# Optimization experiments

Measured on AMD Instinct MI355X. Metric: run time of the kernel, lower is better.

Reference implementation:

```python
import jax, jax.numpy as jnp
import numpy as np

EMBED = 1024
HIDDEN = 4 * EMBED
EPS = 1e-5

def _layer_norm(x, g, b):
    mu = jnp.mean(x, axis=-1, keepdims=True)
    var = jnp.mean((x - mu) ** 2, axis=-1, keepdims=True)
    return (x - mu) * jax.lax.rsqrt(var + EPS) * g + b

def setup_inputs() -> dict:
    key = jax.random.key(0)
    ks = jax.random.split(key, 8)
    s = 1.0 / np.sqrt(EMBED)
    inp = {
        "x": jax.random.normal(ks[0], (4, 2048, EMBED), dtype=jnp.float32),
        "Wq": jax.random.normal(ks[1], (EMBED, EMBED), dtype=jnp.float32) * s,
        "bq": jnp.zeros((EMBED,), jnp.float32),
        "Wk": jax.random.normal(ks[2], (EMBED, EMBED), dtype=jnp.float32) * s,
        "bk": jnp.zeros((EMBED,), jnp.float32),
        "Wv": jax.random.normal(ks[3], (EMBED, EMBED), dtype=jnp.float32) * s,
        "bv": jnp.zeros((EMBED,), jnp.float32),
        "W1": jax.random.normal(ks[4], (EMBED, HIDDEN), dtype=jnp.float32) * s,
        "b1": jnp.zeros((HIDDEN,), jnp.float32),
        "W2": jax.random.normal(ks[5], (HIDDEN, EMBED), dtype=jnp.float32) * (1.0 / np.sqrt(HIDDEN)),
        "b2": jnp.zeros((EMBED,), jnp.float32),
        "g1": jnp.ones((EMBED,), jnp.float32),
        "be1": jnp.zeros((EMBED,), jnp.float32),
        "g2": jnp.ones((EMBED,), jnp.float32),
        "be2": jnp.zeros((EMBED,), jnp.float32),
    }
    return inp

def reference(x, Wq, bq, Wk, bk, Wv, bv, W1, b1, W2, b2, g1, be1, g2, be2):
    # pre-norm attention
    h = _layer_norm(x, g1, be1)
    Q = h @ Wq + bq  # [B,S,D]
    K = h @ Wk + bk
    V = h @ Wv + bv
    scale = 1.0 / jnp.sqrt(jnp.asarray(EMBED, x.dtype))
    scores = jnp.einsum('bqd,bkd->bqk', Q, K) * scale  # [B,S,S]
    weights = jax.nn.softmax(scores, axis=-1)
    attn = jnp.einsum('bqk,bkd->bqd', weights, V)
    x = x + attn
    # pre-norm MLP
    h2 = _layer_norm(x, g2, be2)
    ff = jax.nn.relu(h2 @ W1 + b1) @ W2 + b2
    return x + ff
```

## Files before the change

### kernel.cpp

```cpp
#include <hip/hip_runtime.h>

#define EMBED 1024
#define HID   4096
#define NB    4
#define SEQ   2048

typedef __attribute__((ext_vector_type(8)))  __bf16 bf16x8;
typedef __attribute__((ext_vector_type(4)))  float  f32x4;
typedef __attribute__((ext_vector_type(4)))  int    i32x4;
typedef unsigned short u16;

__device__ __forceinline__ u16 f2bf(float f) {
  unsigned u = __float_as_uint(f);
  u += 0x7FFFu + ((u >> 16) & 1u);
  return (u16)(u >> 16);
}
__device__ __forceinline__ float bf2f(u16 u) {
  return __uint_as_float(((unsigned)u) << 16);
}

typedef const __attribute__((address_space(1))) unsigned int* gas_t;
typedef __attribute__((address_space(3))) unsigned int* las_t;
__device__ __forceinline__ void gld16(const void* g, void* l) {
  __builtin_amdgcn_global_load_lds((gas_t)g, (las_t)l, 16, 0, 0);
}

#define RD16(p)       __builtin_bit_cast(bf16x8, *(const i32x4*)(p))
#define MFMA16(a,b,c) __builtin_amdgcn_mfma_f32_16x16x32_bf16(a, b, c, 0, 0, 0)
#define SCHED0()      __builtin_amdgcn_sched_barrier(0)
#define BARR()        __builtin_amdgcn_s_barrier()
#define LGKM(n)       asm volatile("s_waitcnt lgkmcnt(" #n ")" ::: "memory")
#define VMW(n)        asm volatile("s_waitcnt vmcnt(" #n ")" ::: "memory")

template<int EPI>
__global__ __launch_bounds__(512, 2) void gemm256(
    const u16* __restrict__ A, int lda, long long astr,
    const u16* __restrict__ B, int ldb, long long bstr,
    void* __restrict__ C, int ldc, long long cstr,
    const float* __restrict__ bias,
    const float* __restrict__ add,
    float scale, int Kdim)
{
  __shared__ char lds[131072];

  const int tid  = threadIdx.x;
  const int lane = tid & 63;
  const int w    = tid >> 6;
  const int wr   = w >> 2, wc = w & 3;
  const int l15  = lane & 15, l4 = lane >> 4;

  const int gx   = gridDim.x;
  const int nwg  = gx * gridDim.y;
  const int orig = blockIdx.y * gx + blockIdx.x;
  const int t    = ((nwg & 7) == 0) ? ((orig & 7) * (nwg >> 3) + (orig >> 3)) : orig;
  const int bx   = t % gx, by = t / gx;

  const u16* Ab = A + (size_t)blockIdx.z * astr + (size_t)by * 256 * lda;
  const u16* Bb = B + (size_t)blockIdx.z * bstr + (size_t)bx * 256 * ldb;

  const int    srow = tid >> 3;
  const size_t sa   = (size_t)srow * lda + (size_t)(((tid & 7) ^ (srow & 7)) * 8);
  const size_t sb   = (size_t)srow * ldb + (size_t)(((tid & 7) ^ (srow & 7)) * 8);
  const int    ldst = tid * 16;

  auto stA = [&](int buf, int q, int kk) {
    gld16(Ab + (size_t)(q * 64) * lda + kk + sa, lds + buf * 65536 + q * 8192 + ldst);
  };
  auto stB = [&](int buf, int i, int kk) {
    gld16(Bb + (size_t)(i * 64) * ldb + kk + sb, lds + buf * 65536 + 32768 + i * 8192 + ldst);
  };

  const int arow = (wr * 128 + l15) * 128;
  const int brow = 32768 + (wc * 64 + l15) * 128;
  const int cp0  = ((0 + l4) ^ (l15 & 7)) * 16;
  const int cp1  = ((4 + l4) ^ (l15 & 7)) * 16;

  f32x4 acc[8][4] = {};
  bf16x8 a0, a1, a2, a3, b0, b1, b2, b3, b4, b5, b6, b7;

  const int NT = Kdim >> 6;
  const int NI = NT >> 1;

#define BLOADS(LB) \
    b0 = RD16((LB) + brow + 0 * 2048 + cp0); \
    b1 = RD16((LB) + brow + 1 * 2048 + cp0); \
    b2 = RD16((LB) + brow + 2 * 2048 + cp0); \
    b3 = RD16((LB) + brow + 3 * 2048 + cp0); \
    b4 = RD16((LB) + brow + 0 * 2048 + cp1); \
    b5 = RD16((LB) + brow + 1 * 2048 + cp1); \
    b6 = RD16((LB) + brow + 2 * 2048 + cp1); \
    b7 = RD16((LB) + brow + 3 * 2048 + cp1);

#define PHASE(LB, MP, PRE, STG, VMST) do { \
    a0 = RD16((LB) + arow + (MP) * 4096 + cp0); \
    a1 = RD16((LB) + arow + (MP) * 4096 + cp1); \
    a2 = RD16((LB) + arow + (MP) * 4096 + 2048 + cp0); \
    a3 = RD16((LB) + arow + (MP) * 4096 + 2048 + cp1); \
    PRE STG VMST \
    SCHED0(); BARR(); LGKM(0); SCHED0(); \
    __builtin_amdgcn_s_setprio(1); \
    acc[2*(MP)  ][0] = MFMA16(a0, b0, acc[2*(MP)  ][0]); \
    acc[2*(MP)  ][1] = MFMA16(a0, b1, acc[2*(MP)  ][1]); \
    acc[2*(MP)  ][2] = MFMA16(a0, b2, acc[2*(MP)  ][2]); \
    acc[2*(MP)  ][3] = MFMA16(a0, b3, acc[2*(MP)  ][3]); \
    acc[2*(MP)+1][0] = MFMA16(a2, b0, acc[2*(MP)+1][0]); \
    acc[2*(MP)+1][1] = MFMA16(a2, b1, acc[2*(MP)+1][1]); \
    acc[2*(MP)+1][2] = MFMA16(a2, b2, acc[2*(MP)+1][2]); \
    acc[2*(MP)+1][3] = MFMA16(a2, b3, acc[2*(MP)+1][3]); \
    acc[2*(MP)  ][0] = MFMA16(a1, b4, acc[2*(MP)  ][0]); \
    acc[2*(MP)  ][1] = MFMA16(a1, b5, acc[2*(MP)  ][1]); \
    acc[2*(MP)  ][2] = MFMA16(a1, b6, acc[2*(MP)  ][2]); \
    acc[2*(MP)  ][3] = MFMA16(a1, b7, acc[2*(MP)  ][3]); \
    acc[2*(MP)+1][0] = MFMA16(a3, b4, acc[2*(MP)+1][0]); \
    acc[2*(MP)+1][1] = MFMA16(a3, b5, acc[2*(MP)+1][1]); \
    acc[2*(MP)+1][2] = MFMA16(a3, b6, acc[2*(MP)+1][2]); \
    acc[2*(MP)+1][3] = MFMA16(a3, b7, acc[2*(MP)+1][3]); \
    __builtin_amdgcn_s_setprio(0); \
    SCHED0(); BARR(); SCHED0(); \
  } while (0)

  stB(0, 0, 0); stB(0, 1, 0); stB(0, 2, 0); stB(0, 3, 0);
  stA(0, 0, 0); stA(0, 1, 0); stA(0, 2, 0); stA(0, 3, 0);
  stB(1, 0, 64); stB(1, 1, 64); stB(1, 2, 64); stB(1, 3, 64);
  stA(1, 0, 64); stA(1, 2, 64);
  VMW(6);
  BARR(); SCHED0();

  const char* L0 = lds;
  const char* L1 = lds + 65536;

  for (int I = 0; I < NI; ++I) {
    const bool st = (I + 1 < NI);
    const int k1 = (2 * I + 1) * 64;
    const int k2 = (2 * I + 2) * 64;
    const int k3 = (2 * I + 3) * 64;

    PHASE(L0, 0, BLOADS(L0), { stA(1, 1, k1); stA(1, 3, k1); }, ;);
    PHASE(L0, 1, ;, if (st) { stB(0, 0, k2); stB(0, 1, k2); }, ;);
    PHASE(L0, 2, ;, if (st) { stB(0, 2, k2); stB(0, 3, k2); }, ;);
    if (st) { PHASE(L0, 3, ;, { stA(0, 0, k2); stA(0, 2, k2); }, VMW(6);); }
    else    { PHASE(L0, 3, ;, ;, VMW(0);); }
    PHASE(L1, 0, BLOADS(L1), if (st) { stA(0, 1, k2); stA(0, 3, k2); }, ;);
    PHASE(L1, 1, ;, if (st) { stB(1, 0, k3); stB(1, 1, k3); }, ;);
    PHASE(L1, 2, ;, if (st) { stB(1, 2, k3); stB(1, 3, k3); }, ;);
    if (st) { PHASE(L1, 3, ;, { stA(1, 0, k3); stA(1, 2, k3); }, VMW(6);); }
    else    { PHASE(L1, 3, ;, ;, ;); }
  }
#undef PHASE
#undef BLOADS

  const int bm0 = by * 256 + wr * 128;
  const int bn0 = bx * 256 + wc * 64;
  float* Cf = (float*)C;
  u16*   Ch = (u16*)C;
  #pragma unroll
  for (int mi = 0; mi < 8; ++mi) {
    #pragma unroll
    for (int ni = 0; ni < 4; ++ni) {
      const int col = bn0 + ni * 16 + l15;
      const int r0  = bm0 + mi * 16 + l4 * 4;
      float bv = 0.f;
      if (EPI == 0 || EPI == 3 || EPI == 4) bv = bias[col];
      #pragma unroll
      for (int r = 0; r < 4; ++r) {
        const size_t idx = (size_t)blockIdx.z * cstr + (size_t)(r0 + r) * ldc + col;
        const float v = acc[mi][ni][r];
        if      (EPI == 0) Ch[idx] = f2bf(v + bv);
        else if (EPI == 1) Cf[idx] = v * scale;
        else if (EPI == 3) Ch[idx] = f2bf(fmaxf(v + bv, 0.f));
        else if (EPI == 4) Cf[idx] = v + bv + add[idx];
      }
    }
  }
}

template<int EPI>
__global__ __launch_bounds__(512, 2) void gemm8p(
    const u16* __restrict__ A, int lda, long long astr,
    const u16* __restrict__ B, int ldb, long long bstr,
    void* __restrict__ C, int ldc, long long cstr,
    const float* __restrict__ bias,
    const float* __restrict__ add,
    float scale, int Kdim)
{
  __shared__ i32x4 lds4[9216];
  const int SLOT = 49152;

  const int tid  = threadIdx.x;
  const int lane = tid & 63;
  const int w    = tid >> 6;
  const int wr   = w >> 1, wc = w & 1;
  const int l15  = lane & 15, l4 = lane >> 4;

  const int gx   = gridDim.x;
  const int nwg  = gx * gridDim.y;
  const int orig = blockIdx.y * gx + blockIdx.x;
  const int t    = ((nwg & 7) == 0) ? ((orig & 7) * (nwg >> 3) + (orig >> 3)) : orig;
  const int bx   = t % gx, by = t / gx;

  const u16* Ab = A + (size_t)blockIdx.z * astr + (size_t)by * 256 * lda;
  const u16* Bb = B + (size_t)blockIdx.z * bstr + (size_t)bx * 128 * ldb;

  size_t gaoff[4], gboff[2];
  #pragma unroll
  for (int i = 0; i < 4; ++i) {
    const int idx = i * 512 + tid, row = idx >> 3, gc = (idx & 7) ^ (row & 7);
    gaoff[i] = (size_t)row * lda + gc * 8;
  }
  #pragma unroll
  for (int j = 0; j < 2; ++j) {
    const int idx = j * 512 + tid, row = idx >> 3, gc = (idx & 7) ^ (row & 7);
    gboff[j] = (size_t)row * ldb + gc * 8;
  }

  int aoff[4], boff[4], cp16[2];
  #pragma unroll
  for (int m = 0; m < 4; ++m) aoff[m] = (wr * 64 + m * 16 + l15) * 128;
  #pragma unroll
  for (int n = 0; n < 4; ++n) boff[n] = 32768 + (wc * 64 + n * 16 + l15) * 128;
  cp16[0] = ((0 + l4) ^ (l15 & 7)) * 16;
  cp16[1] = ((4 + l4) ^ (l15 & 7)) * 16;

  f32x4 acc[4][4] = {};
  const int NT = Kdim >> 6;
  char* lbase = (char*)lds4;

  {
    char* s0 = lbase;
    char* s1 = lbase + SLOT;
    #pragma unroll
    for (int i = 0; i < 4; ++i) gld16(Ab + gaoff[i],      s0 + (i * 512 + w * 64) * 16);
    #pragma unroll
    for (int j = 0; j < 2; ++j) gld16(Bb + gboff[j],      s0 + 32768 + (j * 512 + w * 64) * 16);
    #pragma unroll
    for (int i = 0; i < 4; ++i) gld16(Ab + gaoff[i] + 64, s1 + (i * 512 + w * 64) * 16);
    #pragma unroll
    for (int j = 0; j < 2; ++j) gld16(Bb + gboff[j] + 64, s1 + 32768 + (j * 512 + w * 64) * 16);
  }

  int s = 0;
  for (int T = 0; T < NT; ++T) {
    const bool st  = (T + 2 < NT);
    const size_t kk = (size_t)(T + 2) * 64;
    const char* rA = lbase + s * SLOT;
    char* wS = lbase + ((s + 2 >= 3) ? (s - 1) : (s + 2)) * SLOT;

    if (T == NT - 1) VMW(0);
    else             VMW(6);
    BARR();
    SCHED0();

    bf16x8 b0, b1, b2, b3, a0, a1;

    b0 = RD16(rA + boff[0] + cp16[0]);
    b1 = RD16(rA + boff[1] + cp16[0]);
    b2 = RD16(rA + boff[2] + cp16[0]);
    b3 = RD16(rA + boff[3] + cp16[0]);
    a0 = RD16(rA + aoff[0] + cp16[0]);
    a1 = RD16(rA + aoff[1] + cp16[0]);
    if (st) {
      gld16(Ab + gaoff[0] + kk, wS + (0 * 512 + w * 64) * 16);
      gld16(Ab + gaoff[1] + kk, wS + (1 * 512 + w * 64) * 16);
    }
    BARR();
    LGKM(0);
    SCHED0();
    __builtin_amdgcn_s_setprio(1);
    acc[0][0] = MFMA16(a0, b0, acc[0][0]);
    acc[0][1] = MFMA16(a0, b1, acc[0][1]);
    acc[0][2] = MFMA16(a0, b2, acc[0][2]);
    acc[0][3] = MFMA16(a0, b3, acc[0][3]);
    acc[1][0] = MFMA16(a1, b0, acc[1][0]);
    acc[1][1] = MFMA16(a1, b1, acc[1][1]);
    acc[1][2] = MFMA16(a1, b2, acc[1][2]);
    acc[1][3] = MFMA16(a1, b3, acc[1][3]);
    __builtin_amdgcn_s_setprio(0);

    a0 = RD16(rA + aoff[2] + cp16[0]);
    a1 = RD16(rA + aoff[3] + cp16[0]);
    if (st) {
      gld16(Ab + gaoff[2] + kk, wS + (2 * 512 + w * 64) * 16);
      gld16(Ab + gaoff[3] + kk, wS + (3 * 512 + w * 64) * 16);
    }
    BARR();
    LGKM(0);
    SCHED0();
    __builtin_amdgcn_s_setprio(1);
    acc[2][0] = MFMA16(a0, b0, acc[2][0]);
    acc[2][1] = MFMA16(a0, b1, acc[2][1]);
    acc[2][2] = MFMA16(a0, b2, acc[2][2]);
    acc[2][3] = MFMA16(a0, b3, acc[2][3]);
    acc[3][0] = MFMA16(a1, b0, acc[3][0]);
    acc[3][1] = MFMA16(a1, b1, acc[3][1]);
    acc[3][2] = MFMA16(a1, b2, acc[3][2]);
    acc[3][3] = MFMA16(a1, b3, acc[3][3]);
    __builtin_amdgcn_s_setprio(0);

    b0 = RD16(rA + boff[0] + cp16[1]);
    b1 = RD16(rA + boff[1] + cp16[1]);
    b2 = RD16(rA + boff[2] + cp16[1]);
    b3 = RD16(rA + boff[3] + cp16[1]);
    a0 = RD16(rA + aoff[0] + cp16[1]);
    a1 = RD16(rA + aoff[1] + cp16[1]);
    if (st) {
      gld16(Bb + gboff[0] + kk, wS + 32768 + (0 * 512 + w * 64) * 16);
    }
    BARR();
    LGKM(0);
    SCHED0();
    __builtin_amdgcn_s_setprio(1);
    acc[0][0] = MFMA16(a0, b0, acc[0][0]);
    acc[0][1] = MFMA16(a0, b1, acc[0][1]);
    acc[0][2] = MFMA16(a0, b2, acc[0][2]);
    acc[0][3] = MFMA16(a0, b3, acc[0][3]);
    acc[1][0] = MFMA16(a1, b0, acc[1][0]);
    acc[1][1] = MFMA16(a1, b1, acc[1][1]);
    acc[1][2] = MFMA16(a1, b2, acc[1][2]);
    acc[1][3] = MFMA16(a1, b3, acc[1][3]);
    __builtin_amdgcn_s_setprio(0);

    a0 = RD16(rA + aoff[2] + cp16[1]);
    a1 = RD16(rA + aoff[3] + cp16[1]);
    if (st) {
      gld16(Bb + gboff[1] + kk, wS + 32768 + (1 * 512 + w * 64) * 16);
    }
    BARR();
    LGKM(0);
    SCHED0();
    __builtin_amdgcn_s_setprio(1);
    acc[2][0] = MFMA16(a0, b0, acc[2][0]);
    acc[2][1] = MFMA16(a0, b1, acc[2][1]);
    acc[2][2] = MFMA16(a0, b2, acc[2][2]);
    acc[2][3] = MFMA16(a0, b3, acc[2][3]);
    acc[3][0] = MFMA16(a1, b0, acc[3][0]);
    acc[3][1] = MFMA16(a1, b1, acc[3][1]);
    acc[3][2] = MFMA16(a1, b2, acc[3][2]);
    acc[3][3] = MFMA16(a1, b3, acc[3][3]);
    __builtin_amdgcn_s_setprio(0);

    s = (s + 1 == 3) ? 0 : s + 1;
  }

  const int bm0 = by * 256 + wr * 64;
  const int bn0 = bx * 128 + wc * 64;
  float* Cf = (float*)C;
  u16*   Ch = (u16*)C;
  #pragma unroll
  for (int mi = 0; mi < 4; ++mi) {
    #pragma unroll
    for (int ni = 0; ni < 4; ++ni) {
      const int col = bn0 + ni * 16 + l15;
      const int r0  = bm0 + mi * 16 + l4 * 4;
      float bv = 0.f;
      if (EPI == 0 || EPI == 4) bv = bias[col];
      #pragma unroll
      for (int r = 0; r < 4; ++r) {
        const size_t idx = (size_t)blockIdx.z * cstr + (size_t)(r0 + r) * ldc + col;
        const float v = acc[mi][ni][r];
        if      (EPI == 0) Ch[idx] = f2bf(v + bv);
        else if (EPI == 1) Cf[idx] = v * scale;
        else if (EPI == 2) Cf[idx] = v + add[idx];
        else if (EPI == 4) Cf[idx] = v + bv + add[idx];
        else if (EPI == 5) Ch[idx] = f2bf(v + bias[r0 + r]);
        else if (EPI == 6) Ch[idx] = f2bf(v * scale);
      }
    }
  }
}

__global__ __launch_bounds__(256) void ln_kernel(
    const float* __restrict__ x, const float* __restrict__ g,
    const float* __restrict__ be, u16* __restrict__ out)
{
  const int row = blockIdx.x;
  const int tid = threadIdx.x;
  const float4 v = ((const float4*)(x + (size_t)row * EMBED))[tid];
  float s  = v.x + v.y + v.z + v.w;
  float s2 = v.x * v.x + v.y * v.y + v.z * v.z + v.w * v.w;
  #pragma unroll
  for (int m = 1; m < 64; m <<= 1) { s += __shfl_xor(s, m); s2 += __shfl_xor(s2, m); }
  __shared__ float ls[4], ls2[4];
  const int w = tid >> 6;
  if ((tid & 63) == 0) { ls[w] = s; ls2[w] = s2; }
  __syncthreads();
  s  = ls[0] + ls[1] + ls[2] + ls[3];
  s2 = ls2[0] + ls2[1] + ls2[2] + ls2[3];
  const float mu   = s * (1.f / EMBED);
  const float var  = s2 * (1.f / EMBED) - mu * mu;
  const float rstd = rsqrtf(var + 1e-5f);
  const float4 gv = ((const float4*)g)[tid];
  const float4 bv = ((const float4*)be)[tid];
  ushort4 o;
  o.x = f2bf((v.x - mu) * rstd * gv.x + bv.x);
  o.y = f2bf((v.y - mu) * rstd * gv.y + bv.y);
  o.z = f2bf((v.z - mu) * rstd * gv.z + bv.z);
  o.w = f2bf((v.w - mu) * rstd * gv.w + bv.w);
  ((ushort4*)(out + (size_t)row * EMBED))[tid] = o;
}

__global__ __launch_bounds__(256) void softmax_bf16(
    const u16* __restrict__ S, u16* __restrict__ P)
{
  const int tid = threadIdx.x;
  const size_t base = ((size_t)blockIdx.y * SEQ + blockIdx.x) * SEQ;
  const ushort4* src = (const ushort4*)(S + base);
  const ushort4 ua = src[tid];
  const ushort4 ub = src[tid + 256];
  float a0 = bf2f(ua.x), a1 = bf2f(ua.y), a2 = bf2f(ua.z), a3 = bf2f(ua.w);
  float b0 = bf2f(ub.x), b1 = bf2f(ub.y), b2 = bf2f(ub.z), b3 = bf2f(ub.w);
  float m = fmaxf(fmaxf(fmaxf(a0, a1), fmaxf(a2, a3)),
                  fmaxf(fmaxf(b0, b1), fmaxf(b2, b3)));
  #pragma unroll
  for (int msk = 1; msk < 64; msk <<= 1) m = fmaxf(m, __shfl_xor(m, msk));
  __shared__ float red[8];
  const int w = tid >> 6;
  if ((tid & 63) == 0) red[w] = m;
  __syncthreads();
  m = fmaxf(fmaxf(red[0], red[1]), fmaxf(red[2], red[3]));
  a0 = __expf(a0 - m); a1 = __expf(a1 - m); a2 = __expf(a2 - m); a3 = __expf(a3 - m);
  b0 = __expf(b0 - m); b1 = __expf(b1 - m); b2 = __expf(b2 - m); b3 = __expf(b3 - m);
  float s = a0 + a1 + a2 + a3 + b0 + b1 + b2 + b3;
  #pragma unroll
  for (int msk = 1; msk < 64; msk <<= 1) s += __shfl_xor(s, msk);
  if ((tid & 63) == 0) red[4 + w] = s;
  __syncthreads();
  s = red[4] + red[5] + red[6] + red[7];
  const float inv = 1.0f / s;
  ushort4 oa, ob;
  oa.x = f2bf(a0 * inv); oa.y = f2bf(a1 * inv); oa.z = f2bf(a2 * inv); oa.w = f2bf(a3 * inv);
  ob.x = f2bf(b0 * inv); ob.y = f2bf(b1 * inv); ob.z = f2bf(b2 * inv); ob.w = f2bf(b3 * inv);
  ushort4* dst = (ushort4*)(P + base);
  dst[tid]       = oa;
  dst[tid + 256] = ob;
}

__global__ void transpose_cast3(const float* __restrict__ W0,
                                const float* __restrict__ W1_,
                                const float* __restrict__ W2_,
                                u16* __restrict__ Wt)
{
  __shared__ float t[32][33];
  const int z = blockIdx.z;
  const float* W = (z == 0) ? W0 : (z == 1) ? W1_ : W2_;
  u16* dst = Wt + (size_t)z * EMBED * EMBED;
  const int tx = threadIdx.x, ty = threadIdx.y;
  const int n0 = blockIdx.x * 32, k0 = blockIdx.y * 32;
  #pragma unroll
  for (int i = 0; i < 4; ++i)
    t[ty + i * 8][tx] = W[(size_t)(k0 + ty + i * 8) * EMBED + n0 + tx];
  __syncthreads();
  #pragma unroll
  for (int i = 0; i < 4; ++i)
    dst[(size_t)(n0 + ty + i * 8) * EMBED + k0 + tx] = f2bf(t[tx][ty + i * 8]);
}

__global__ void transpose_cast_f32(const float* __restrict__ W, u16* __restrict__ Wt,
                                   int K, int N)
{
  __shared__ float t[32][33];
  const int tx = threadIdx.x, ty = threadIdx.y;
  const int n0 = blockIdx.x * 32, k0 = blockIdx.y * 32;
  #pragma unroll
  for (int i = 0; i < 4; ++i)
    t[ty + i * 8][tx] = W[(size_t)(k0 + ty + i * 8) * N + n0 + tx];
  __syncthreads();
  #pragma unroll
  for (int i = 0; i < 4; ++i)
    Wt[(size_t)(n0 + ty + i * 8) * K + k0 + tx] = f2bf(t[tx][ty + i * 8]);
}

__global__ void concat_bias2(const float* __restrict__ a, const float* __restrict__ b,
                             float* __restrict__ o)
{
  const int i = blockIdx.x * 1024 + threadIdx.x;
  o[i] = (i < 1024) ? a[i] : b[i - 1024];
}

extern "C" void kernel_launch(void* const* d_in, const int* in_sizes, int n_in,
                              void* d_out, int out_size, void* d_ws, size_t ws_size,
                              hipStream_t stream)
{
  const float* x   = (const float*)d_in[0];
  const float* Wq  = (const float*)d_in[1];
  const float* bq  = (const float*)d_in[2];
  const float* Wk  = (const float*)d_in[3];
  const float* bk  = (const float*)d_in[4];
  const float* Wv  = (const float*)d_in[5];
  const float* bv  = (const float*)d_in[6];
  const float* W1  = (const float*)d_in[7];
  const float* b1  = (const float*)d_in[8];
  const float* W2  = (const float*)d_in[9];
  const float* b2  = (const float*)d_in[10];
  const float* g1  = (const float*)d_in[11];
  const float* be1 = (const float*)d_in[12];
  const float* g2  = (const float*)d_in[13];
  const float* be2 = (const float*)d_in[14];
  float* out = (float*)d_out;

  const size_t RD = (size_t)NB * SEQ * EMBED;

  char* base = (char*)d_ws;
  size_t o = 0;
  auto alloc = [&](size_t bytes) -> void* {
    o = (o + 255) & ~(size_t)255;
    void* p = base + o;
    o += bytes;
    return p;
  };

  u16*   wqkv3T = (u16*)alloc((size_t)3 * EMBED * EMBED * 2);
  u16*   w1T    = (u16*)alloc((size_t)HID * EMBED * 2);
  u16*   w2T    = (u16*)alloc((size_t)EMBED * HID * 2);
  float* bqk    = (float*)alloc(2048 * 4);
  u16*   h      = (u16*)alloc(RD * 2);
  u16*   QKb    = (u16*)alloc(RD * 2 * 2);
  u16*   Vt     = (u16*)alloc(RD * 2);
  float* x2     = (float*)alloc(RD * 4);

  const size_t need_batched = o + (size_t)NB * SEQ * SEQ * 4 + 1024;
  const int NZ = (ws_size >= need_batched) ? NB : 1;
  u16* Sb16 = (u16*)alloc((size_t)NZ * SEQ * SEQ * 2);
  u16* Pb   = (u16*)alloc((size_t)NZ * SEQ * SEQ * 2);
  u16* ff   = (NZ == NB) ? Sb16
                         : (u16*)alloc((size_t)NB * SEQ * HID * 2);

  const u16* wqkT = wqkv3T;
  const u16* wvT  = wqkv3T + (size_t)2 * EMBED * EMBED;

  const dim3 blk(512);
  const dim3 tblk(32, 8);

  transpose_cast3<<<dim3(32, 32, 3), tblk, 0, stream>>>(Wq, Wk, Wv, wqkv3T);
  transpose_cast_f32<<<dim3(HID / 32, EMBED / 32), tblk, 0, stream>>>(W1, w1T, EMBED, HID);
  transpose_cast_f32<<<dim3(EMBED / 32, HID / 32), tblk, 0, stream>>>(W2, w2T, HID, EMBED);
  concat_bias2<<<dim3(2), dim3(1024), 0, stream>>>(bq, bk, bqk);

  ln_kernel<<<dim3(NB * SEQ), dim3(256), 0, stream>>>(x, g1, be1, h);

  gemm8p<0><<<dim3(2048 / 128, NB * SEQ / 256, 1), blk, 0, stream>>>(
      h, EMBED, 0LL, wqkT, EMBED, 0LL, QKb, 2048, 0LL, bqk, nullptr, 1.f, EMBED);

  gemm8p<5><<<dim3(SEQ / 128, EMBED / 256, NB), blk, 0, stream>>>(
      wvT, EMBED, 0LL, h, EMBED, (long long)SEQ * EMBED,
      Vt, SEQ, (long long)EMBED * SEQ, bv, nullptr, 1.f, EMBED);

  for (int b = 0; b < NB; b += NZ) {
    const u16* Qp  = QKb + (size_t)b * SEQ * 2048;
    const u16* Kp  = Qp + 1024;
    const u16* Vtp = Vt + (size_t)b * EMBED * SEQ;
    float* x2p     = x2 + (size_t)b * SEQ * EMBED;
    const float* xp = x + (size_t)b * SEQ * EMBED;
    gemm8p<6><<<dim3(SEQ / 128, SEQ / 256, NZ), blk, 0, stream>>>(
        Qp, 2048, (long long)SEQ * 2048, Kp, 2048, (long long)SEQ * 2048,
        Sb16, SEQ, (long long)SEQ * SEQ, nullptr, nullptr, 0.03125f, EMBED);
    softmax_bf16<<<dim3(SEQ, NZ), dim3(256), 0, stream>>>(Sb16, Pb);
    gemm8p<2><<<dim3(EMBED / 128, SEQ / 256, NZ), blk, 0, stream>>>(
        Pb, SEQ, (long long)SEQ * SEQ, Vtp, SEQ, (long long)EMBED * SEQ,
        x2p, EMBED, (long long)SEQ * EMBED, nullptr, xp, 1.f, SEQ);
  }

  ln_kernel<<<dim3(NB * SEQ), dim3(256), 0, stream>>>(x2, g2, be2, h);

  gemm256<3><<<dim3(HID / 256, NB * SEQ / 256, 1), blk, 0, stream>>>(
      h, EMBED, 0LL, w1T, EMBED, 0LL, ff, HID, 0LL, b1, nullptr, 1.f, EMBED);
  gemm8p<4><<<dim3(EMBED / 128, NB * SEQ / 256, 1), blk, 0, stream>>>(
      ff, HID, 0LL, w2T, HID, 0LL, out, EMBED, 0LL, b2, x2, 1.f, HID);
}
```

Measured before the change: 333.0 us.

## Simplify 256x256 GEMM pipeline and use it for QK projection and scores

Replaces the hand-interleaved 8-phase ping-pong main loop of the 256x256 GEMM with a simpler double-buffered loop. Each iteration waits for all loads, barriers once, issues the next tile's global-to-LDS loads, then software-pipelines the A-fragment LDS reads against MFMAs. The kernel gains a scaled bf16 epilogue and now also runs the QK projection and the QK^T score GEMMs, which previously used the 128-wide gemm8p kernel. This is meant to raise per-block data reuse with larger output tiles, at the cost of a full vmcnt(0) wait each k-step that may expose global load latency.

```diff
diff --git a/kernel.cpp b/kernel.cpp
--- a/kernel.cpp
+++ b/kernel.cpp
@@ -33,12 +33,11 @@
 #define VMW(n)        asm volatile("s_waitcnt vmcnt(" #n ")" ::: "memory")
 
 template<int EPI>
-__global__ __launch_bounds__(512, 2) void gemm256(
+__global__ __launch_bounds__(512, 2) void gemm256v3(
     const u16* __restrict__ A, int lda, long long astr,
     const u16* __restrict__ B, int ldb, long long bstr,
     void* __restrict__ C, int ldc, long long cstr,
     const float* __restrict__ bias,
-    const float* __restrict__ add,
     float scale, int Kdim)
 {
   __shared__ char lds[131072];
@@ -76,83 +75,72 @@
   const int cp1  = ((4 + l4) ^ (l15 & 7)) * 16;
 
   f32x4 acc[8][4] = {};
-  bf16x8 a0, a1, a2, a3, b0, b1, b2, b3, b4, b5, b6, b7;
-
   const int NT = Kdim >> 6;
-  const int NI = NT >> 1;
-
-#define BLOADS(LB) \
-    b0 = RD16((LB) + brow + 0 * 2048 + cp0); \
-    b1 = RD16((LB) + brow + 1 * 2048 + cp0); \
-    b2 = RD16((LB) + brow + 2 * 2048 + cp0); \
-    b3 = RD16((LB) + brow + 3 * 2048 + cp0); \
-    b4 = RD16((LB) + brow + 0 * 2048 + cp1); \
-    b5 = RD16((LB) + brow + 1 * 2048 + cp1); \
-    b6 = RD16((LB) + brow + 2 * 2048 + cp1); \
-    b7 = RD16((LB) + brow + 3 * 2048 + cp1);
-
-#define PHASE(LB, MP, PRE, STG, VMST) do { \
-    a0 = RD16((LB) + arow + (MP) * 4096 + cp0); \
-    a1 = RD16((LB) + arow + (MP) * 4096 + cp1); \
-    a2 = RD16((LB) + arow + (MP) * 4096 + 2048 + cp0); \
-    a3 = RD16((LB) + arow + (MP) * 4096 + 2048 + cp1); \
-    PRE STG VMST \
-    SCHED0(); BARR(); LGKM(0); SCHED0(); \
-    __builtin_amdgcn_s_setprio(1); \
-    acc[2*(MP)  ][0] = MFMA16(a0, b0, acc[2*(MP)  ][0]); \
-    acc[2*(MP)  ][1] = MFMA16(a0, b1, acc[2*(MP)  ][1]); \
-    acc[2*(MP)  ][2] = MFMA16(a0, b2, acc[2*(MP)  ][2]); \
-    acc[2*(MP)  ][3] = MFMA16(a0, b3, acc[2*(MP)  ][3]); \
-    acc[2*(MP)+1][0] = MFMA16(a2, b0, acc[2*(MP)+1][0]); \
-    acc[2*(MP)+1][1] = MFMA16(a2, b1, acc[2*(MP)+1][1]); \
-    acc[2*(MP)+1][2] = MFMA16(a2, b2, acc[2*(MP)+1][2]); \
-    acc[2*(MP)+1][3] = MFMA16(a2, b3, acc[2*(MP)+1][3]); \
-    acc[2*(MP)  ][0] = MFMA16(a1, b4, acc[2*(MP)  ][0]); \
-    acc[2*(MP)  ][1] = MFMA16(a1, b5, acc[2*(MP)  ][1]); \
-    acc[2*(MP)  ][2] = MFMA16(a1, b6, acc[2*(MP)  ][2]); \
-    acc[2*(MP)  ][3] = MFMA16(a1, b7, acc[2*(MP)  ][3]); \
-    acc[2*(MP)+1][0] = MFMA16(a3, b4, acc[2*(MP)+1][0]); \
-    acc[2*(MP)+1][1] = MFMA16(a3, b5, acc[2*(MP)+1][1]); \
-    acc[2*(MP)+1][2] = MFMA16(a3, b6, acc[2*(MP)+1][2]); \
-    acc[2*(MP)+1][3] = MFMA16(a3, b7, acc[2*(MP)+1][3]); \
-    __builtin_amdgcn_s_setprio(0); \
-    SCHED0(); BARR(); SCHED0(); \
-  } while (0)
 
   stB(0, 0, 0); stB(0, 1, 0); stB(0, 2, 0); stB(0, 3, 0);
   stA(0, 0, 0); stA(0, 1, 0); stA(0, 2, 0); stA(0, 3, 0);
-  stB(1, 0, 64); stB(1, 1, 64); stB(1, 2, 64); stB(1, 3, 64);
-  stA(1, 0, 64); stA(1, 2, 64);
-  VMW(6);
-  BARR(); SCHED0();
-
-  const char* L0 = lds;
-  const char* L1 = lds + 65536;
-
-  for (int I = 0; I < NI; ++I) {
-    const bool st = (I + 1 < NI);
-    const int k1 = (2 * I + 1) * 64;
-    const int k2 = (2 * I + 2) * 64;
-    const int k3 = (2 * I + 3) * 64;
-
-    PHASE(L0, 0, BLOADS(L0), { stA(1, 1, k1); stA(1, 3, k1); }, ;);
-    PHASE(L0, 1, ;, if (st) { stB(0, 0, k2); stB(0, 1, k2); }, ;);
-    PHASE(L0, 2, ;, if (st) { stB(0, 2, k2); stB(0, 3, k2); }, ;);
-    if (st) { PHASE(L0, 3, ;, { stA(0, 0, k2); stA(0, 2, k2); }, VMW(6);); }
-    else    { PHASE(L0, 3, ;, ;, VMW(0);); }
-    PHASE(L1, 0, BLOADS(L1), if (st) { stA(0, 1, k2); stA(0, 3, k2); }, ;);
-    PHASE(L1, 1, ;, if (st) { stB(1, 0, k3); stB(1, 1, k3); }, ;);
-    PHASE(L1, 2, ;, if (st) { stB(1, 2, k3); stB(1, 3, k3); }, ;);
-    if (st) { PHASE(L1, 3, ;, { stA(1, 0, k3); stA(1, 2, k3); }, VMW(6);); }
-    else    { PHASE(L1, 3, ;, ;, ;); }
-  }
-#undef PHASE
-#undef BLOADS
+
+  for (int T = 0; T < NT; ++T) {
+    const char* LB = lds + (T & 1) * 65536;
+    VMW(0);
+    SCHED0();
+    BARR();
+    SCHED0();
+
+    if (T + 1 < NT) {
+      const int b = (T & 1) ^ 1, kk = (T + 1) * 64;
+      stB(b, 0, kk); stB(b, 1, kk); stB(b, 2, kk); stB(b, 3, kk);
+      stA(b, 0, kk); stA(b, 1, kk); stA(b, 2, kk); stA(b, 3, kk);
+    }
+
+    bf16x8 b0 = RD16(LB + brow + 0 * 2048 + cp0);
+    bf16x8 b1 = RD16(LB + brow + 1 * 2048 + cp0);
+    bf16x8 b2 = RD16(LB + brow + 2 * 2048 + cp0);
+    bf16x8 b3 = RD16(LB + brow + 3 * 2048 + cp0);
+    bf16x8 b4 = RD16(LB + brow + 0 * 2048 + cp1);
+    bf16x8 b5 = RD16(LB + brow + 1 * 2048 + cp1);
+    bf16x8 b6 = RD16(LB + brow + 2 * 2048 + cp1);
+    bf16x8 b7 = RD16(LB + brow + 3 * 2048 + cp1);
+
+#define AQ(MP, x0, x1, x2, x3) \
+    bf16x8 x0 = RD16(LB + arow + (MP) * 4096 + cp0); \
+    bf16x8 x1 = RD16(LB + arow + (MP) * 4096 + cp1); \
+    bf16x8 x2 = RD16(LB + arow + (MP) * 4096 + 2048 + cp0); \
+    bf16x8 x3 = RD16(LB + arow + (MP) * 4096 + 2048 + cp1);
+
+#define MQ(MP, x0, x1, x2, x3) \
+    acc[2*(MP)  ][0] = MFMA16(x0, b0, acc[2*(MP)  ][0]); \
+    acc[2*(MP)  ][1] = MFMA16(x0, b1, acc[2*(MP)  ][1]); \
+    acc[2*(MP)  ][2] = MFMA16(x0, b2, acc[2*(MP)  ][2]); \
+    acc[2*(MP)  ][3] = MFMA16(x0, b3, acc[2*(MP)  ][3]); \
+    acc[2*(MP)+1][0] = MFMA16(x2, b0, acc[2*(MP)+1][0]); \
+    acc[2*(MP)+1][1] = MFMA16(x2, b1, acc[2*(MP)+1][1]); \
+    acc[2*(MP)+1][2] = MFMA16(x2, b2, acc[2*(MP)+1][2]); \
+    acc[2*(MP)+1][3] = MFMA16(x2, b3, acc[2*(MP)+1][3]); \
+    acc[2*(MP)  ][0] = MFMA16(x1, b4, acc[2*(MP)  ][0]); \
+    acc[2*(MP)  ][1] = MFMA16(x1, b5, acc[2*(MP)  ][1]); \
+    acc[2*(MP)  ][2] = MFMA16(x1, b6, acc[2*(MP)  ][2]); \
+    acc[2*(MP)  ][3] = MFMA16(x1, b7, acc[2*(MP)  ][3]); \
+    acc[2*(MP)+1][0] = MFMA16(x3, b4, acc[2*(MP)+1][0]); \
+    acc[2*(MP)+1][1] = MFMA16(x3, b5, acc[2*(MP)+1][1]); \
+    acc[2*(MP)+1][2] = MFMA16(x3, b6, acc[2*(MP)+1][2]); \
+    acc[2*(MP)+1][3] = MFMA16(x3, b7, acc[2*(MP)+1][3]);
+
+    AQ(0, a00, a01, a02, a03)
+    AQ(1, a10, a11, a12, a13)
+    MQ(0, a00, a01, a02, a03)
+    AQ(2, a20, a21, a22, a23)
+    MQ(1, a10, a11, a12, a13)
+    AQ(3, a30, a31, a32, a33)
+    MQ(2, a20, a21, a22, a23)
+    MQ(3, a30, a31, a32, a33)
+#undef AQ
+#undef MQ
+  }
 
   const int bm0 = by * 256 + wr * 128;
   const int bn0 = bx * 256 + wc * 64;
-  float* Cf = (float*)C;
-  u16*   Ch = (u16*)C;
+  u16* Ch = (u16*)C;
   #pragma unroll
   for (int mi = 0; mi < 8; ++mi) {
     #pragma unroll
@@ -160,15 +148,14 @@
       const int col = bn0 + ni * 16 + l15;
       const int r0  = bm0 + mi * 16 + l4 * 4;
       float bv = 0.f;
-      if (EPI == 0 || EPI == 3 || EPI == 4) bv = bias[col];
+      if (EPI == 0 || EPI == 3) bv = bias[col];
       #pragma unroll
       for (int r = 0; r < 4; ++r) {
         const size_t idx = (size_t)blockIdx.z * cstr + (size_t)(r0 + r) * ldc + col;
         const float v = acc[mi][ni][r];
         if      (EPI == 0) Ch[idx] = f2bf(v + bv);
-        else if (EPI == 1) Cf[idx] = v * scale;
         else if (EPI == 3) Ch[idx] = f2bf(fmaxf(v + bv, 0.f));
-        else if (EPI == 4) Cf[idx] = v + bv + add[idx];
+        else if (EPI == 6) Ch[idx] = f2bf(v * scale);
       }
     }
   }
@@ -537,8 +524,8 @@
 
   ln_kernel<<<dim3(NB * SEQ), dim3(256), 0, stream>>>(x, g1, be1, h);
 
-  gemm8p<0><<<dim3(2048 / 128, NB * SEQ / 256, 1), blk, 0, stream>>>(
-      h, EMBED, 0LL, wqkT, EMBED, 0LL, QKb, 2048, 0LL, bqk, nullptr, 1.f, EMBED);
+  gemm256v3<0><<<dim3(2048 / 256, NB * SEQ / 256, 1), blk, 0, stream>>>(
+      h, EMBED, 0LL, wqkT, EMBED, 0LL, QKb, 2048, 0LL, bqk, 1.f, EMBED);
 
   gemm8p<5><<<dim3(SEQ / 128, EMBED / 256, NB), blk, 0, stream>>>(
       wvT, EMBED, 0LL, h, EMBED, (long long)SEQ * EMBED,
@@ -550,9 +537,9 @@
     const u16* Vtp = Vt + (size_t)b * EMBED * SEQ;
     float* x2p     = x2 + (size_t)b * SEQ * EMBED;
     const float* xp = x + (size_t)b * SEQ * EMBED;
-    gemm8p<6><<<dim3(SEQ / 128, SEQ / 256, NZ), blk, 0, stream>>>(
+    gemm256v3<6><<<dim3(SEQ / 256, SEQ / 256, NZ), blk, 0, stream>>>(
         Qp, 2048, (long long)SEQ * 2048, Kp, 2048, (long long)SEQ * 2048,
-        Sb16, SEQ, (long long)SEQ * SEQ, nullptr, nullptr, 0.03125f, EMBED);
+        Sb16, SEQ, (long long)SEQ * SEQ, nullptr, 0.03125f, EMBED);
     softmax_bf16<<<dim3(SEQ, NZ), dim3(256), 0, stream>>>(Sb16, Pb);
     gemm8p<2><<<dim3(EMBED / 128, SEQ / 256, NZ), blk, 0, stream>>>(
         Pb, SEQ, (long long)SEQ * SEQ, Vtp, SEQ, (long long)EMBED * SEQ,
@@ -561,8 +548,8 @@
 
   ln_kernel<<<dim3(NB * SEQ), dim3(256), 0, stream>>>(x2, g2, be2, h);
 
-  gemm256<3><<<dim3(HID / 256, NB * SEQ / 256, 1), blk, 0, stream>>>(
-      h, EMBED, 0LL, w1T, EMBED, 0LL, ff, HID, 0LL, b1, nullptr, 1.f, EMBED);
+  gemm256v3<3><<<dim3(HID / 256, NB * SEQ / 256, 1), blk, 0, stream>>>(
+      h, EMBED, 0LL, w1T, EMBED, 0LL, ff, HID, 0LL, b1, 1.f, EMBED);
   gemm8p<4><<<dim3(EMBED / 128, NB * SEQ / 256, 1), blk, 0, stream>>>(
       ff, HID, 0LL, w2T, HID, 0LL, out, EMBED, 0LL, b2, x2, 1.f, HID);
 }
```

After: 321.9 us. 1.03x faster.
